# Kernel optimization log

Hardware: AMD Instinct MI355X
Metric: run time of the kernel (lower is better)

Reference implementation:

```python
import jax, jax.numpy as jnp
import numpy as np

DEPTH, HEADS, DIM_HEAD = 6, 8, 64
B, N, E = 2, 128, 160
NUM_ATOMS, NF = 100, 127
DIM = NF + 1                 # 128, node feature dim fed to transformer
INNER = HEADS * DIM_HEAD     # 512


def setup_inputs() -> dict:
    key = jax.random.key(0)
    ks = iter(jax.random.split(key, 40))
    f32 = jnp.float32
    def w(shape, scale=0.02):
        return jax.random.normal(next(ks), shape, dtype=f32) * scale
    inp = {
        "indices": jax.random.randint(next(ks), (B, N), 0, NUM_ATOMS),
        "coordinates": jax.random.normal(next(ks), (B, N, 3), dtype=f32),
        "bonds": jax.random.randint(next(ks), (E, 2), 0, N),
        "noise_level": jax.random.uniform(next(ks), (1,), dtype=f32),
        "atom_emb": w((NUM_ATOMS, NF), 1.0),
        "ln1_g": jnp.ones((DEPTH, DIM), f32), "ln1_b": jnp.zeros((DEPTH, DIM), f32),
        "Wq": w((DEPTH, DIM, INNER)), "bq": jnp.zeros((DEPTH, INNER), f32),
        "Wkv": w((DEPTH, DIM, 2 * INNER)), "bkv": jnp.zeros((DEPTH, 2 * INNER), f32),
        "We": w((DEPTH, 3, INNER)), "be": jnp.zeros((DEPTH, INNER), f32),
        "Wo": w((DEPTH, INNER, DIM)), "bo": jnp.zeros((DEPTH, DIM), f32),
        "Wg1": w((DEPTH, 3 * DIM, 1)),
        "ln2_g": jnp.ones((DEPTH, DIM), f32), "ln2_b": jnp.zeros((DEPTH, DIM), f32),
        "W1": w((DEPTH, DIM, 4 * DIM)), "b1": jnp.zeros((DEPTH, 4 * DIM), f32),
        "W2": w((DEPTH, 4 * DIM, DIM)), "b2": jnp.zeros((DEPTH, DIM), f32),
        "Wg2": w((DEPTH, 3 * DIM, 1)),
        "Wlin": w((DIM, 1)), "blin": jnp.zeros((1,), f32),
    }
    return inp


def _ln(x, g, b, eps=1e-5):
    m = jnp.mean(x, -1, keepdims=True)
    v = jnp.mean((x - m) ** 2, -1, keepdims=True)
    return (x - m) * jax.lax.rsqrt(v + eps) * g + b


def _gated_residual(x, res, Wg):
    # gate = sigmoid(Linear([x, res, x-res])); out = x*gate + res*(1-gate)
    gate = jax.nn.sigmoid(jnp.concatenate([x, res, x - res], -1) @ Wg)  # (B,N,1)
    return x * gate + res * (1.0 - gate)


def _forward(indices, bonds, coordinates, noise_level, atom_emb,
             ln1_g, ln1_b, Wq, bq, Wkv, bkv, We, be, Wo, bo, Wg1,
             ln2_g, ln2_b, W1, b1, W2, b2, Wg2, Wlin, blin):
    b, n = indices.shape
    # nodes_embedding: atom embedding + noise-level channel
    noise = jnp.broadcast_to(noise_level.reshape(1, 1, 1).astype(coordinates.dtype), (b, n, 1))
    nodes = jnp.concatenate([atom_emb[indices], noise], -1)  # (B,N,DIM)
    # edges_embedding: vectorized scatter of per-bond coordinate differences
    i, j = bonds[:, 0], bonds[:, 1]
    diff = coordinates[:, i] - coordinates[:, j]             # (B,E,3)
    edges = jnp.zeros((b, n, n, 3), coordinates.dtype)
    edges = edges.at[:, i, j].set(diff).at[:, j, i].set(-diff)

    scale = DIM_HEAD ** -0.5
    for l in range(DEPTH):
        # PreNorm + edge-biased attention (mask is all-ones -> no-op)
        xn = _ln(nodes, ln1_g[l], ln1_b[l])
        q = (xn @ Wq[l] + bq[l]).reshape(b, n, HEADS, DIM_HEAD)
        k, v = jnp.split(xn @ Wkv[l] + bkv[l], 2, -1)
        k = k.reshape(b, n, HEADS, DIM_HEAD)
        v = v.reshape(b, n, HEADS, DIM_HEAD)
        e = (edges @ We[l] + be[l]).reshape(b, n, n, HEADS, DIM_HEAD)
        kk = k[:, None] + e                                   # (B,i,j,H,D)
        vv = v[:, None] + e
        sim = jnp.einsum('bihd,bijhd->bijh', q, kk) * scale
        attn = jax.nn.softmax(sim, axis=2)                    # softmax over j
        out = jnp.einsum('bijh,bijhd->bihd', attn, vv).reshape(b, n, INNER)
        out = out @ Wo[l] + bo[l]
        nodes = _gated_residual(out, nodes, Wg1[l])
        # PreNorm + FeedForward (exact GELU, mult=4) + gated residual
        xn = _ln(nodes, ln2_g[l], ln2_b[l])
        ff = jax.nn.gelu(xn @ W1[l] + b1[l], approximate=False) @ W2[l] + b2[l]
        nodes = _gated_residual(ff, nodes, Wg2[l])
    return jnp.sum(nodes @ Wlin + blin)


def reference(indices, coordinates, bonds, noise_level, atom_emb,
              ln1_g, ln1_b, Wq, bq, Wkv, bkv, We, be, Wo, bo, Wg1,
              ln2_g, ln2_b, W1, b1, W2, b2, Wg2, Wlin, blin):
    return _forward(indices, bonds, coordinates, noise_level, atom_emb,
                    ln1_g, ln1_b, Wq, bq, Wkv, bkv, We, be, Wo, bo, Wg1,
                    ln2_g, ln2_b, W1, b1, W2, b2, Wg2, Wlin, blin)
```

## Files before the change

kernel.cpp:

```cpp
#include <hip/hip_runtime.h>
#include <hip/hip_fp16.h>
#include <math.h>

#define DEPTH 6
#define HEADS 8
#define BB    2
#define NN    128
#define EE    160
#define NF    127
#define DIMM  128
#define INNER 512
#define NNODE 256

__device__ __forceinline__ void gload16(const void* g, void* l) {
    __builtin_amdgcn_global_load_lds((const __attribute__((address_space(1))) void*)g,
                                     (__attribute__((address_space(3))) void*)l,
                                     16, 0, 0);
}

__device__ __forceinline__ void wait_vm0() { __builtin_amdgcn_s_waitcnt(0x0f70); }
__device__ __forceinline__ void wait_lgkm0() { __builtin_amdgcn_s_waitcnt(0xC07F); }

__device__ __forceinline__ void wstage16(const char* gslice, char* ldsslice, int ln) {
#pragma unroll
    for (int i = 0; i < 16; i++)
        gload16(gslice + i * 1024 + ln * 16, ldsslice + i * 1024);
}
__device__ __forceinline__ void wstage16s(const char* gslice, int rowstride,
                                          char* ldsslice, int ln) {
#pragma unroll
    for (int i = 0; i < 16; i++)
        gload16(gslice + (size_t)i * rowstride + ln * 16, ldsslice + i * 1024);
}

__device__ __forceinline__ void fma8h(float4& a0, float4& a1, float s, float4 raw) {
    const __half2* hp = (const __half2*)&raw;
    float2 p0 = __half22float2(hp[0]), p1 = __half22float2(hp[1]);
    float2 p2 = __half22float2(hp[2]), p3 = __half22float2(hp[3]);
    a0.x += s * p0.x; a0.y += s * p0.y; a0.z += s * p1.x; a0.w += s * p1.y;
    a1.x += s * p2.x; a1.y += s * p2.y; a1.z += s * p3.x; a1.w += s * p3.y;
}

__device__ __forceinline__ void gemv512(const float* act, const float* wbuf,
                                        float* s_part, int w, int ln) {
    float4 a0 = {0,0,0,0}, a1 = {0,0,0,0};
    const float4* w4 = (const float4*)wbuf;
#pragma unroll
    for (int r = 0; r < 16; r++)
        fma8h(a0, a1, act[w * 16 + r], w4[r * 64 + ln]);
    ((float4*)(s_part + w * 512))[ln * 2]     = a0;
    ((float4*)(s_part + w * 512))[ln * 2 + 1] = a1;
}

__device__ __forceinline__ void gemv128(const float* act, const float* wbuf,
                                        float* s_part, int w, int ln) {
    float2 acc = {0, 0};
#pragma unroll 8
    for (int r = 0; r < 64; r++) {
        float raw = wbuf[r * 64 + ln];
        float2 p = __half22float2(*(const __half2*)&raw);
        float a = act[w * 64 + r];
        acc.x += a * p.x; acc.y += a * p.y;
    }
    s_part[w * 128 + ln * 2]     = acc.x;
    s_part[w * 128 + ln * 2 + 1] = acc.y;
}

template <int N>
__device__ __forceinline__ void block_reduce_n(float* vals, float* sbuf) {
#pragma unroll
    for (int off = 32; off > 0; off >>= 1)
#pragma unroll
        for (int q = 0; q < N; q++) vals[q] += __shfl_xor(vals[q], off, 64);
    int wave = threadIdx.x >> 6;
    if ((threadIdx.x & 63) == 0)
#pragma unroll
        for (int q = 0; q < N; q++) sbuf[wave * N + q] = vals[q];
    __syncthreads();
#pragma unroll
    for (int q = 0; q < N; q++) {
        float r = 0.0f;
#pragma unroll
        for (int g = 0; g < 8; g++) r += sbuf[g * N + q];
        vals[q] = r;
    }
    __syncthreads();
}

__device__ __forceinline__ float gelu_exact(float a) {
    return 0.5f * a * (1.0f + erff(a * 0.70710678f));
}


__global__ __launch_bounds__(512) void k_cvt(const float* Wq, const float* Wkv,
                                             const float* Wo, const float* W1,
                                             const float* W2,
                                             __half* hWq, __half* hWkv, __half* hWo,
                                             __half* hW1, __half* hW2,
                                             const float* blin, float* out) {
    if (blockIdx.x == 0 && threadIdx.x == 0) out[0] = 256.0f * blin[0];
    int g = blockIdx.x * 512 + threadIdx.x;
    const float4* src; __half* dst; int off;
    if (g < 98304)       { src = (const float4*)Wq;  dst = hWq;  off = g; }
    else if (g < 294912) { src = (const float4*)Wkv; dst = hWkv; off = g - 98304; }
    else if (g < 393216) { src = (const float4*)Wo;  dst = hWo;  off = g - 294912; }
    else if (g < 491520) { src = (const float4*)W1;  dst = hW1;  off = g - 393216; }
    else                 { src = (const float4*)W2;  dst = hW2;  off = g - 491520; }
    float4 v = src[off];
    __half2* d2 = (__half2*)(dst + (size_t)off * 4);
    d2[0] = __floats2half2_rn(v.x, v.y);
    d2[1] = __floats2half2_rn(v.z, v.w);
}

__global__ __launch_bounds__(512, 1) void k_pre(const int* indices, const float* noise,
                                                const float* atom_emb,
                                                const float* ln1_g, const float* ln1_b,
                                                const __half* hWq, const float* bq,
                                                const __half* hWkv, const float* bkv,
                                                float* nodes, float* qb,
                                                __half* hk, __half* hv) {
    int bn = blockIdx.x;
    int t  = threadIdx.x;
    int d  = t & 127;
    bool own = (t < 128);
    int w = t >> 6, ln = t & 63;
    __shared__ float arena[32768];
    __shared__ float s_xn[128];
    __shared__ float s_red[48];
    __shared__ float s_part[4096];
    char*  lslice = (char*)arena + w * 16384;
    float* wbuf   = arena + w * 4096;

    const char* WqL  = (const char*)hWq;
    const char* WkvL = (const char*)hWkv;
    wstage16(WqL + w * 16384, lslice, ln);

    float nd = 0.0f;
    if (own) {
        int idx = indices[bn];
        nd = (d < NF) ? atom_emb[idx * NF + d] : noise[0];
        nodes[bn * DIMM + d] = nd;
    }
    float vals[2] = {own ? nd : 0.0f, own ? nd * nd : 0.0f};
    block_reduce_n<2>(vals, s_red);
    float m   = vals[0] * (1.0f / 128.0f);
    float var = vals[1] * (1.0f / 128.0f) - m * m;
    if (own) s_xn[d] = (nd - m) * rsqrtf(var + 1e-5f) * ln1_g[d] + ln1_b[d];
    __syncthreads();

    wait_vm0();
    gemv512(s_xn, wbuf, s_part, w, ln);
    wait_lgkm0();
    wstage16s(WkvL + (size_t)(w * 16) * 2048, 2048, lslice, ln);
    __syncthreads();
    {
        float q = bq[t];
#pragma unroll
        for (int g = 0; g < 8; g++) q += s_part[g * 512 + t];
        qb[(size_t)bn * INNER + t] = q;
    }
    __syncthreads();

    wait_vm0();
    gemv512(s_xn, wbuf, s_part, w, ln);
    wait_lgkm0();
    wstage16s(WkvL + (size_t)(w * 16) * 2048 + 1024, 2048, lslice, ln);
    __syncthreads();
    {
        float k = bkv[t];
#pragma unroll
        for (int g = 0; g < 8; g++) k += s_part[g * 512 + t];
        hk[(size_t)bn * INNER + t] = __float2half(k);
    }
    __syncthreads();

    wait_vm0();
    gemv512(s_xn, wbuf, s_part, w, ln);
    __syncthreads();
    {
        float v = bkv[INNER + t];
#pragma unroll
        for (int g = 0; g < 8; g++) v += s_part[g * 512 + t];
        hv[(size_t)bn * INNER + t] = __float2half(v);
    }
}

__global__ __launch_bounds__(512, 1) void k_layer(int l,
        const float* coords, const int* bonds,
        const float* We, const float* be,
        float* qb, const __half* hkin, const __half* hvin,
        __half* hkout, __half* hvout,
        const __half* hWo, const float* bo, const float* Wg1,
        const float* ln2_g, const float* ln2_b,
        const __half* hW1, const float* b1,
        const __half* hW2, const float* b2,
        const float* Wg2,
        const float* ln1_g, const float* ln1_b,
        const __half* hWq, const float* bq,
        const __half* hWkv, const float* bkv,
        float* nodes, const float* Wlin, float* out) {
    int bn = blockIdx.x;
    int b = bn >> 7, i = bn & 127;
    int t = threadIdx.x;
    int d = t & 127;
    bool own = (t < 128);
    int w = t >> 6, ln = t & 63;

    __shared__ float arena[32768];
    __shared__ float scoord[384];
    __shared__ float sedge[384];
    __shared__ int   sadj[128];
    __shared__ float s_l[64];
    __shared__ float s_ao[512];
    __shared__ float s_h[512];
    __shared__ float s_xn[128];
    __shared__ float s_red[48];
    __shared__ float s_part[4096];
    float* s_o = s_part;
    char*  lslice = (char*)arena + w * 16384;
    float* wbuf   = arena + w * 4096;

    const char* WoL  = (const char*)(hWo + (size_t)l * INNER * DIMM);
    const char* W1L  = (const char*)(hW1 + (size_t)l * DIMM * 4 * DIMM);
    const char* W2L  = (const char*)(hW2 + (size_t)l * 4 * DIMM * DIMM);
    const char* WqL  = (const char*)(hWq + (size_t)(l + 1) * DIMM * INNER);
    const char* WkvL = (const char*)(hWkv + (size_t)(l + 1) * DIMM * 2 * INNER);

    wstage16(WoL + w * 16384, lslice, ln);

    const float4* qR4 = (const float4*)(qb + (size_t)bn * INNER);
    const float4* WeR = (const float4*)(We + (size_t)l * 3 * INNER);
    float4 qa  = qR4[ln * 2],        qz  = qR4[ln * 2 + 1];
    float4 w0a = WeR[ln * 2],        w0z = WeR[ln * 2 + 1];
    float4 w1a = WeR[128 + ln * 2],  w1z = WeR[129 + ln * 2];
    float4 w2a = WeR[256 + ln * 2],  w2z = WeR[257 + ln * 2];
    float4 bea = ((const float4*)(be + (size_t)l * INNER))[ln * 2];
    float4 bez = ((const float4*)(be + (size_t)l * INNER))[ln * 2 + 1];
    float res = own ? nodes[bn * DIMM + d] : 0.0f;

    if (t < 3 * NN) scoord[t] = coords[b * 3 * NN + t];
    if (t < NN) sadj[t] = 0;
    __syncthreads();
    if (t < EE) {
        int e0 = bonds[2 * t], e1 = bonds[2 * t + 1];
        if (e0 == i) sadj[e1] = 1;
        if (e1 == i) sadj[e0] = 1;
    }
    __syncthreads();
    if (t < NN) {
        int j = t;
        float msk = sadj[j] ? 1.0f : 0.0f;
        sedge[3 * j + 0] = msk * (scoord[3 * i + 0] - scoord[3 * j + 0]);
        sedge[3 * j + 1] = msk * (scoord[3 * i + 1] - scoord[3 * j + 1]);
        sedge[3 * j + 2] = msk * (scoord[3 * i + 2] - scoord[3 * j + 2]);
    }
    __syncthreads();

    const float4* kR = (const float4*)(hkin + (size_t)b * NN * INNER);
    const float4* vR = (const float4*)(hvin + (size_t)b * NN * INNER);
    float l_run = 0.0f;
    float4 o0 = {0, 0, 0, 0}, o1 = {0, 0, 0, 0};
    int j0 = w * 16;
#pragma unroll
    for (int base = 0; base < 16; base += 4) {
        float4 kraw[4], vraw[4];
#pragma unroll
        for (int p = 0; p < 4; p++) {
            int j = j0 + base + p;
            kraw[p] = kR[j * 64 + ln];
            vraw[p] = vR[j * 64 + ln];
        }
#pragma unroll
        for (int p = 0; p < 4; p++) {
            int j = j0 + base + p;
            float ex = sedge[3 * j], ey = sedge[3 * j + 1], ez = sedge[3 * j + 2];
            float4 e0, e1;
            e0.x = bea.x + ex * w0a.x + ey * w1a.x + ez * w2a.x;
            e0.y = bea.y + ex * w0a.y + ey * w1a.y + ez * w2a.y;
            e0.z = bea.z + ex * w0a.z + ey * w1a.z + ez * w2a.z;
            e0.w = bea.w + ex * w0a.w + ey * w1a.w + ez * w2a.w;
            e1.x = bez.x + ex * w0z.x + ey * w1z.x + ez * w2z.x;
            e1.y = bez.y + ex * w0z.y + ey * w1z.y + ez * w2z.y;
            e1.z = bez.z + ex * w0z.z + ey * w1z.z + ez * w2z.z;
            e1.w = bez.w + ex * w0z.w + ey * w1z.w + ez * w2z.w;
            const __half2* kh = (const __half2*)&kraw[p];
            float2 k0 = __half22float2(kh[0]), k1 = __half22float2(kh[1]);
            float2 k2 = __half22float2(kh[2]), k3 = __half22float2(kh[3]);
            float s = qa.x * (k0.x + e0.x) + qa.y * (k0.y + e0.y)
                    + qa.z * (k1.x + e0.z) + qa.w * (k1.y + e0.w)
                    + qz.x * (k2.x + e1.x) + qz.y * (k2.y + e1.y)
                    + qz.z * (k3.x + e1.z) + qz.w * (k3.y + e1.w);
            s += __shfl_xor(s, 1, 64);
            s += __shfl_xor(s, 2, 64);
            s += __shfl_xor(s, 4, 64);
            float pp = __expf(s * 0.125f);
            const __half2* vh = (const __half2*)&vraw[p];
            float2 v0 = __half22float2(vh[0]), v1 = __half22float2(vh[1]);
            float2 v2 = __half22float2(vh[2]), v3 = __half22float2(vh[3]);
            l_run += pp;
            o0.x += pp * (v0.x + e0.x); o0.y += pp * (v0.y + e0.y);
            o0.z += pp * (v1.x + e0.z); o0.w += pp * (v1.y + e0.w);
            o1.x += pp * (v2.x + e1.x); o1.y += pp * (v2.y + e1.y);
            o1.z += pp * (v3.x + e1.z); o1.w += pp * (v3.y + e1.w);
        }
    }
    ((float4*)(s_o + w * 512))[ln * 2]     = o0;
    ((float4*)(s_o + w * 512))[ln * 2 + 1] = o1;
    if ((ln & 7) == 0) s_l[w * 8 + (ln >> 3)] = l_run;
    __syncthreads();
    {
        float o = 0.0f;
#pragma unroll
        for (int g = 0; g < 8; g++) o += s_o[g * 512 + t];
        int h = t >> 6;
        float lsum = 0.0f;
#pragma unroll
        for (int g = 0; g < 8; g++) lsum += s_l[g * 8 + h];
        s_ao[t] = o / lsum;
    }
    __syncthreads();

    wait_vm0();
    gemv128(s_ao, wbuf, s_part, w, ln);
    wait_lgkm0();
    wstage16(W1L + w * 16384, lslice, ln);
    __syncthreads();
    float x = 0.0f;
    if (own) {
        x = bo[l * DIMM + d];
#pragma unroll
        for (int g = 0; g < 8; g++) x += s_part[g * 128 + d];
    }

    const float* Wg1_l = Wg1 + l * 3 * DIMM;
    float n1;
    {
        float tex = own ? (x * Wg1_l[d] + res * Wg1_l[DIMM + d] + (x - res) * Wg1_l[2 * DIMM + d]) : 0.0f;
        float vals[6] = {tex,
                         own ? x : 0.0f, own ? x * x : 0.0f,
                         own ? x * res : 0.0f,
                         own ? res : 0.0f, own ? res * res : 0.0f};
        block_reduce_n<6>(vals, s_red);
        float g1 = 1.0f / (1.0f + __expf(-vals[0]));
        float sn  = g1 * vals[1] + (1.0f - g1) * vals[4];
        float sn2 = g1 * g1 * vals[2] + 2.0f * g1 * (1.0f - g1) * vals[3]
                  + (1.0f - g1) * (1.0f - g1) * vals[5];
        float m   = sn * (1.0f / 128.0f);
        float var = sn2 * (1.0f / 128.0f) - m * m;
        n1 = x * g1 + res * (1.0f - g1);
        if (own) s_xn[d] = (n1 - m) * rsqrtf(var + 1e-5f) * ln2_g[l * DIMM + d] + ln2_b[l * DIMM + d];
    }
    __syncthreads();

    wait_vm0();
    gemv512(s_xn, wbuf, s_part, w, ln);
    wait_lgkm0();
    wstage16(W2L + w * 16384, lslice, ln);
    __syncthreads();
    {
        float a = b1[l * 4 * DIMM + t];
#pragma unroll
        for (int g = 0; g < 8; g++) a += s_part[g * 512 + t];
        s_h[t] = gelu_exact(a);
    }
    __syncthreads();

    wait_vm0();
    gemv128(s_h, wbuf, s_part, w, ln);
    wait_lgkm0();
    if (l < DEPTH - 1) wstage16(WqL + w * 16384, lslice, ln);
    __syncthreads();
    float y = 0.0f;
    if (own) {
        y = b2[l * DIMM + d];
#pragma unroll
        for (int g = 0; g < 8; g++) y += s_part[g * 128 + d];
    }

    const float* Wg2_l = Wg2 + l * 3 * DIMM;
    if (l < DEPTH - 1) {
        float tex = own ? (y * Wg2_l[d] + n1 * Wg2_l[DIMM + d] + (y - n1) * Wg2_l[2 * DIMM + d]) : 0.0f;
        float vals[6] = {tex,
                         own ? y : 0.0f, own ? y * y : 0.0f,
                         own ? y * n1 : 0.0f,
                         own ? n1 : 0.0f, own ? n1 * n1 : 0.0f};
        block_reduce_n<6>(vals, s_red);
        float g2 = 1.0f / (1.0f + __expf(-vals[0]));
        float sn  = g2 * vals[1] + (1.0f - g2) * vals[4];
        float sn2 = g2 * g2 * vals[2] + 2.0f * g2 * (1.0f - g2) * vals[3]
                  + (1.0f - g2) * (1.0f - g2) * vals[5];
        float m   = sn * (1.0f / 128.0f);
        float var = sn2 * (1.0f / 128.0f) - m * m;
        float n2 = y * g2 + n1 * (1.0f - g2);
        if (own) {
            nodes[bn * DIMM + d] = n2;
            s_xn[d] = (n2 - m) * rsqrtf(var + 1e-5f) * ln1_g[(l + 1) * DIMM + d]
                    + ln1_b[(l + 1) * DIMM + d];
        }
        __syncthreads();

        wait_vm0();
        gemv512(s_xn, wbuf, s_part, w, ln);
        wait_lgkm0();
        wstage16s(WkvL + (size_t)(w * 16) * 2048, 2048, lslice, ln);
        __syncthreads();
        {
            float q = bq[(l + 1) * INNER + t];
#pragma unroll
            for (int g = 0; g < 8; g++) q += s_part[g * 512 + t];
            qb[(size_t)bn * INNER + t] = q;
        }
        __syncthreads();

        wait_vm0();
        gemv512(s_xn, wbuf, s_part, w, ln);
        wait_lgkm0();
        wstage16s(WkvL + (size_t)(w * 16) * 2048 + 1024, 2048, lslice, ln);
        __syncthreads();
        {
            float k = bkv[(l + 1) * 2 * INNER + t];
#pragma unroll
            for (int g = 0; g < 8; g++) k += s_part[g * 512 + t];
            hkout[(size_t)bn * INNER + t] = __float2half(k);
        }
        __syncthreads();

        wait_vm0();
        gemv512(s_xn, wbuf, s_part, w, ln);
        __syncthreads();
        {
            float v = bkv[(l + 1) * 2 * INNER + INNER + t];
#pragma unroll
            for (int g = 0; g < 8; g++) v += s_part[g * 512 + t];
            hvout[(size_t)bn * INNER + t] = __float2half(v);
        }
    } else {
        float wl = own ? Wlin[d] : 0.0f;
        float tex = own ? (y * Wg2_l[d] + n1 * Wg2_l[DIMM + d] + (y - n1) * Wg2_l[2 * DIMM + d]) : 0.0f;
        float vals[3] = {tex, y * wl, n1 * wl};
        block_reduce_n<3>(vals, s_red);
        float g2 = 1.0f / (1.0f + __expf(-vals[0]));
        float tot = g2 * vals[1] + (1.0f - g2) * vals[2];
        if (t == 0) atomicAdd(out, tot);
    }
}

extern "C" void kernel_launch(void* const* d_in, const int* in_sizes, int n_in,
                              void* d_out, int out_size, void* d_ws, size_t ws_size,
                              hipStream_t stream) {
    const int*   indices = (const int*)d_in[0];
    const float* coords  = (const float*)d_in[1];
    const int*   bonds   = (const int*)d_in[2];
    const float* noise   = (const float*)d_in[3];
    const float* atom_emb= (const float*)d_in[4];
    const float* ln1_g   = (const float*)d_in[5];
    const float* ln1_b   = (const float*)d_in[6];
    const float* Wq      = (const float*)d_in[7];
    const float* bq      = (const float*)d_in[8];
    const float* Wkv     = (const float*)d_in[9];
    const float* bkv     = (const float*)d_in[10];
    const float* We      = (const float*)d_in[11];
    const float* be      = (const float*)d_in[12];
    const float* Wo      = (const float*)d_in[13];
    const float* bo      = (const float*)d_in[14];
    const float* Wg1     = (const float*)d_in[15];
    const float* ln2_g   = (const float*)d_in[16];
    const float* ln2_b   = (const float*)d_in[17];
    const float* W1      = (const float*)d_in[18];
    const float* b1      = (const float*)d_in[19];
    const float* W2      = (const float*)d_in[20];
    const float* b2      = (const float*)d_in[21];
    const float* Wg2     = (const float*)d_in[22];
    const float* Wlin    = (const float*)d_in[23];
    const float* blin    = (const float*)d_in[24];

    float*  ws    = (float*)d_ws;
    float*  nodes = ws;
    float*  qb    = nodes + NNODE * DIMM;
    __half* hkb   = (__half*)(qb + NNODE * INNER);
    __half* hvb   = hkb + 2 * NNODE * INNER;
    __half* hWq   = hvb + 2 * NNODE * INNER;
    __half* hWkv  = hWq + DEPTH * DIMM * INNER;
    __half* hWo   = hWkv + DEPTH * DIMM * 2 * INNER;
    __half* hW1   = hWo + DEPTH * INNER * DIMM;
    __half* hW2   = hW1 + DEPTH * DIMM * 4 * DIMM;

    k_cvt<<<1152, 512, 0, stream>>>(Wq, Wkv, Wo, W1, W2, hWq, hWkv, hWo, hW1, hW2,
                                    blin, (float*)d_out);
    k_pre<<<NNODE, 512, 0, stream>>>(indices, noise, atom_emb, ln1_g, ln1_b,
                                     hWq, bq, hWkv, bkv, nodes, qb, hkb, hvb);
    for (int l = 0; l < DEPTH; l++) {
        const __half* hkin = hkb + (size_t)(l & 1) * NNODE * INNER;
        const __half* hvin = hvb + (size_t)(l & 1) * NNODE * INNER;
        __half* hkout = hkb + (size_t)((l + 1) & 1) * NNODE * INNER;
        __half* hvout = hvb + (size_t)((l + 1) & 1) * NNODE * INNER;
        k_layer<<<NNODE, 512, 0, stream>>>(l, coords, bonds, We, be,
                                           qb, hkin, hvin, hkout, hvout,
                                           hWo, bo, Wg1, ln2_g, ln2_b, hW1, b1, hW2, b2,
                                           Wg2, ln1_g, ln1_b, hWq, bq, hWkv, bkv,
                                           nodes, Wlin, (float*)d_out);
    }
}
```

Baseline: 270.1 us.

## Fuse all layers into one persistent kernel with grid barriers

Replaces the pre-kernel and six per-layer launches with a single persistent kernel of 256 blocks that loops over layers and synchronises with a software grid barrier on atomics. Node state and q now stay in registers and shared memory instead of round-tripping through global memory, and the next layer's Wo is prefetched during the QKV phase. The attention score switches to packed fp16 dot products (fdot2), and the edge term is skipped for unbonded pairs using a precomputed q·bias constant. The changes aim to cut launch overhead and redundant edge arithmetic. The barrier relies on all 256 blocks being co-resident, and q is rounded to fp16 for the score.

```diff
diff --git a/kernel.cpp b/kernel.cpp
--- a/kernel.cpp
+++ b/kernel.cpp
@@ -11,6 +11,23 @@
 #define DIMM  128
 #define INNER 512
 #define NNODE 256
+#define NBLK  256
+
+typedef _Float16 h2f16 __attribute__((ext_vector_type(2)));
+
+#if defined(__has_builtin)
+#if __has_builtin(__builtin_amdgcn_fdot2)
+#define HAVE_FDOT2 1
+#endif
+#endif
+
+__device__ __forceinline__ float fdot2f(h2f16 a, h2f16 b, float c) {
+#ifdef HAVE_FDOT2
+    return __builtin_amdgcn_fdot2(a, b, c, false);
+#else
+    return c + (float)a.x * (float)b.x + (float)a.y * (float)b.y;
+#endif
+}
 
 __device__ __forceinline__ void gload16(const void* g, void* l) {
     __builtin_amdgcn_global_load_lds((const __attribute__((address_space(1))) void*)g,
@@ -91,14 +108,37 @@
     return 0.5f * a * (1.0f + erff(a * 0.70710678f));
 }
 
+__device__ __forceinline__ void gridbar(unsigned* bar) {
+    __syncthreads();
+    if (threadIdx.x == 0) {
+        __threadfence();
+        unsigned g = __hip_atomic_load(&bar[1], __ATOMIC_RELAXED, __HIP_MEMORY_SCOPE_AGENT);
+        unsigned a = __hip_atomic_fetch_add(&bar[0], 1u, __ATOMIC_ACQ_REL, __HIP_MEMORY_SCOPE_AGENT);
+        if (a == NBLK - 1) {
+            __hip_atomic_store(&bar[0], 0u, __ATOMIC_RELAXED, __HIP_MEMORY_SCOPE_AGENT);
+            __hip_atomic_fetch_add(&bar[1], 1u, __ATOMIC_RELEASE, __HIP_MEMORY_SCOPE_AGENT);
+        } else {
+            while (__hip_atomic_load(&bar[1], __ATOMIC_ACQUIRE, __HIP_MEMORY_SCOPE_AGENT) == g)
+                __builtin_amdgcn_s_sleep(2);
+        }
+        __threadfence();
+    }
+    __syncthreads();
+}
+
 
 __global__ __launch_bounds__(512) void k_cvt(const float* Wq, const float* Wkv,
                                              const float* Wo, const float* W1,
                                              const float* W2,
                                              __half* hWq, __half* hWkv, __half* hWo,
                                              __half* hW1, __half* hW2,
-                                             const float* blin, float* out) {
-    if (blockIdx.x == 0 && threadIdx.x == 0) out[0] = 256.0f * blin[0];
+                                             const float* blin, float* out,
+                                             unsigned* bar) {
+    if (blockIdx.x == 0 && threadIdx.x == 0) {
+        out[0] = 256.0f * blin[0];
+        bar[0] = 0u;
+        bar[1] = 0u;
+    }
     int g = blockIdx.x * 512 + threadIdx.x;
     const float4* src; __half* dst; int off;
     if (g < 98304)       { src = (const float4*)Wq;  dst = hWq;  off = g; }
@@ -112,52 +152,22 @@
     d2[1] = __floats2half2_rn(v.z, v.w);
 }
 
-__global__ __launch_bounds__(512, 1) void k_pre(const int* indices, const float* noise,
-                                                const float* atom_emb,
-                                                const float* ln1_g, const float* ln1_b,
-                                                const __half* hWq, const float* bq,
-                                                const __half* hWkv, const float* bkv,
-                                                float* nodes, float* qb,
-                                                __half* hk, __half* hv) {
-    int bn = blockIdx.x;
-    int t  = threadIdx.x;
-    int d  = t & 127;
-    bool own = (t < 128);
-    int w = t >> 6, ln = t & 63;
-    __shared__ float arena[32768];
-    __shared__ float s_xn[128];
-    __shared__ float s_red[48];
-    __shared__ float s_part[4096];
-    char*  lslice = (char*)arena + w * 16384;
-    float* wbuf   = arena + w * 4096;
-
-    const char* WqL  = (const char*)hWq;
-    const char* WkvL = (const char*)hWkv;
-    wstage16(WqL + w * 16384, lslice, ln);
-
-    float nd = 0.0f;
-    if (own) {
-        int idx = indices[bn];
-        nd = (d < NF) ? atom_emb[idx * NF + d] : noise[0];
-        nodes[bn * DIMM + d] = nd;
-    }
-    float vals[2] = {own ? nd : 0.0f, own ? nd * nd : 0.0f};
-    block_reduce_n<2>(vals, s_red);
-    float m   = vals[0] * (1.0f / 128.0f);
-    float var = vals[1] * (1.0f / 128.0f) - m * m;
-    if (own) s_xn[d] = (nd - m) * rsqrtf(var + 1e-5f) * ln1_g[d] + ln1_b[d];
-    __syncthreads();
-
+__device__ __forceinline__ void qkv_phase(const float* s_xn, float* s_part, float* s_q,
+                                          char* lslice, float* wbuf,
+                                          const char* WkvL, const char* WoNextL,
+                                          const float* bq_l, const float* bkv_l,
+                                          __half* hkrow, __half* hvrow,
+                                          int w, int ln, int t) {
     wait_vm0();
     gemv512(s_xn, wbuf, s_part, w, ln);
     wait_lgkm0();
     wstage16s(WkvL + (size_t)(w * 16) * 2048, 2048, lslice, ln);
     __syncthreads();
     {
-        float q = bq[t];
+        float q = bq_l[t];
 #pragma unroll
         for (int g = 0; g < 8; g++) q += s_part[g * 512 + t];
-        qb[(size_t)bn * INNER + t] = q;
+        s_q[t] = q;
     }
     __syncthreads();
 
@@ -167,38 +177,36 @@
     wstage16s(WkvL + (size_t)(w * 16) * 2048 + 1024, 2048, lslice, ln);
     __syncthreads();
     {
-        float k = bkv[t];
+        float k = bkv_l[t];
 #pragma unroll
         for (int g = 0; g < 8; g++) k += s_part[g * 512 + t];
-        hk[(size_t)bn * INNER + t] = __float2half(k);
+        hkrow[t] = __float2half(k);
     }
     __syncthreads();
 
     wait_vm0();
     gemv512(s_xn, wbuf, s_part, w, ln);
+    wait_lgkm0();
+    wstage16(WoNextL + w * 16384, lslice, ln);
     __syncthreads();
     {
-        float v = bkv[INNER + t];
+        float v = bkv_l[INNER + t];
 #pragma unroll
         for (int g = 0; g < 8; g++) v += s_part[g * 512 + t];
-        hv[(size_t)bn * INNER + t] = __float2half(v);
-    }
-}
-
-__global__ __launch_bounds__(512, 1) void k_layer(int l,
-        const float* coords, const int* bonds,
+        hvrow[t] = __float2half(v);
+    }
+}
+
+__global__ __launch_bounds__(512, 1) void k_net(
+        const int* indices, const float* coords, const int* bonds, const float* noise,
+        const float* atom_emb, const float* ln1_g, const float* ln1_b,
+        const __half* hWq, const float* bq, const __half* hWkv, const float* bkv,
         const float* We, const float* be,
-        float* qb, const __half* hkin, const __half* hvin,
-        __half* hkout, __half* hvout,
         const __half* hWo, const float* bo, const float* Wg1,
         const float* ln2_g, const float* ln2_b,
-        const __half* hW1, const float* b1,
-        const __half* hW2, const float* b2,
-        const float* Wg2,
-        const float* ln1_g, const float* ln1_b,
-        const __half* hWq, const float* bq,
-        const __half* hWkv, const float* bkv,
-        float* nodes, const float* Wlin, float* out) {
+        const __half* hW1, const float* b1, const __half* hW2, const float* b2,
+        const float* Wg2, const float* Wlin, float* out,
+        __half* hkb, __half* hvb, unsigned* bar) {
     int bn = blockIdx.x;
     int b = bn >> 7, i = bn & 127;
     int t = threadIdx.x;
@@ -216,27 +224,12 @@
     __shared__ float s_xn[128];
     __shared__ float s_red[48];
     __shared__ float s_part[4096];
+    __shared__ float s_q[512];
     float* s_o = s_part;
     char*  lslice = (char*)arena + w * 16384;
     float* wbuf   = arena + w * 4096;
 
-    const char* WoL  = (const char*)(hWo + (size_t)l * INNER * DIMM);
-    const char* W1L  = (const char*)(hW1 + (size_t)l * DIMM * 4 * DIMM);
-    const char* W2L  = (const char*)(hW2 + (size_t)l * 4 * DIMM * DIMM);
-    const char* WqL  = (const char*)(hWq + (size_t)(l + 1) * DIMM * INNER);
-    const char* WkvL = (const char*)(hWkv + (size_t)(l + 1) * DIMM * 2 * INNER);
-
-    wstage16(WoL + w * 16384, lslice, ln);
-
-    const float4* qR4 = (const float4*)(qb + (size_t)bn * INNER);
-    const float4* WeR = (const float4*)(We + (size_t)l * 3 * INNER);
-    float4 qa  = qR4[ln * 2],        qz  = qR4[ln * 2 + 1];
-    float4 w0a = WeR[ln * 2],        w0z = WeR[ln * 2 + 1];
-    float4 w1a = WeR[128 + ln * 2],  w1z = WeR[129 + ln * 2];
-    float4 w2a = WeR[256 + ln * 2],  w2z = WeR[257 + ln * 2];
-    float4 bea = ((const float4*)(be + (size_t)l * INNER))[ln * 2];
-    float4 bez = ((const float4*)(be + (size_t)l * INNER))[ln * 2 + 1];
-    float res = own ? nodes[bn * DIMM + d] : 0.0f;
+    wstage16((const char*)hWq + w * 16384, lslice, ln);
 
     if (t < 3 * NN) scoord[t] = coords[b * 3 * NN + t];
     if (t < NN) sadj[t] = 0;
@@ -254,194 +247,216 @@
         sedge[3 * j + 1] = msk * (scoord[3 * i + 1] - scoord[3 * j + 1]);
         sedge[3 * j + 2] = msk * (scoord[3 * i + 2] - scoord[3 * j + 2]);
     }
-    __syncthreads();
-
-    const float4* kR = (const float4*)(hkin + (size_t)b * NN * INNER);
-    const float4* vR = (const float4*)(hvin + (size_t)b * NN * INNER);
-    float l_run = 0.0f;
-    float4 o0 = {0, 0, 0, 0}, o1 = {0, 0, 0, 0};
-    int j0 = w * 16;
-#pragma unroll
-    for (int base = 0; base < 16; base += 4) {
-        float4 kraw[4], vraw[4];
-#pragma unroll
-        for (int p = 0; p < 4; p++) {
-            int j = j0 + base + p;
-            kraw[p] = kR[j * 64 + ln];
-            vraw[p] = vR[j * 64 + ln];
-        }
-#pragma unroll
-        for (int p = 0; p < 4; p++) {
-            int j = j0 + base + p;
-            float ex = sedge[3 * j], ey = sedge[3 * j + 1], ez = sedge[3 * j + 2];
-            float4 e0, e1;
-            e0.x = bea.x + ex * w0a.x + ey * w1a.x + ez * w2a.x;
-            e0.y = bea.y + ex * w0a.y + ey * w1a.y + ez * w2a.y;
-            e0.z = bea.z + ex * w0a.z + ey * w1a.z + ez * w2a.z;
-            e0.w = bea.w + ex * w0a.w + ey * w1a.w + ez * w2a.w;
-            e1.x = bez.x + ex * w0z.x + ey * w1z.x + ez * w2z.x;
-            e1.y = bez.y + ex * w0z.y + ey * w1z.y + ez * w2z.y;
-            e1.z = bez.z + ex * w0z.z + ey * w1z.z + ez * w2z.z;
-            e1.w = bez.w + ex * w0z.w + ey * w1z.w + ez * w2z.w;
-            const __half2* kh = (const __half2*)&kraw[p];
-            float2 k0 = __half22float2(kh[0]), k1 = __half22float2(kh[1]);
-            float2 k2 = __half22float2(kh[2]), k3 = __half22float2(kh[3]);
-            float s = qa.x * (k0.x + e0.x) + qa.y * (k0.y + e0.y)
-                    + qa.z * (k1.x + e0.z) + qa.w * (k1.y + e0.w)
-                    + qz.x * (k2.x + e1.x) + qz.y * (k2.y + e1.y)
-                    + qz.z * (k3.x + e1.z) + qz.w * (k3.y + e1.w);
-            s += __shfl_xor(s, 1, 64);
-            s += __shfl_xor(s, 2, 64);
-            s += __shfl_xor(s, 4, 64);
-            float pp = __expf(s * 0.125f);
-            const __half2* vh = (const __half2*)&vraw[p];
-            float2 v0 = __half22float2(vh[0]), v1 = __half22float2(vh[1]);
-            float2 v2 = __half22float2(vh[2]), v3 = __half22float2(vh[3]);
-            l_run += pp;
-            o0.x += pp * (v0.x + e0.x); o0.y += pp * (v0.y + e0.y);
-            o0.z += pp * (v1.x + e0.z); o0.w += pp * (v1.y + e0.w);
-            o1.x += pp * (v2.x + e1.x); o1.y += pp * (v2.y + e1.y);
-            o1.z += pp * (v3.x + e1.z); o1.w += pp * (v3.y + e1.w);
-        }
-    }
-    ((float4*)(s_o + w * 512))[ln * 2]     = o0;
-    ((float4*)(s_o + w * 512))[ln * 2 + 1] = o1;
-    if ((ln & 7) == 0) s_l[w * 8 + (ln >> 3)] = l_run;
-    __syncthreads();
+
+    float res = 0.0f;
+    if (own) {
+        int idx = indices[bn];
+        res = (d < NF) ? atom_emb[idx * NF + d] : noise[0];
+    }
     {
-        float o = 0.0f;
-#pragma unroll
-        for (int g = 0; g < 8; g++) o += s_o[g * 512 + t];
-        int h = t >> 6;
-        float lsum = 0.0f;
-#pragma unroll
-        for (int g = 0; g < 8; g++) lsum += s_l[g * 8 + h];
-        s_ao[t] = o / lsum;
-    }
-    __syncthreads();
-
-    wait_vm0();
-    gemv128(s_ao, wbuf, s_part, w, ln);
-    wait_lgkm0();
-    wstage16(W1L + w * 16384, lslice, ln);
-    __syncthreads();
-    float x = 0.0f;
-    if (own) {
-        x = bo[l * DIMM + d];
-#pragma unroll
-        for (int g = 0; g < 8; g++) x += s_part[g * 128 + d];
-    }
-
-    const float* Wg1_l = Wg1 + l * 3 * DIMM;
-    float n1;
-    {
-        float tex = own ? (x * Wg1_l[d] + res * Wg1_l[DIMM + d] + (x - res) * Wg1_l[2 * DIMM + d]) : 0.0f;
-        float vals[6] = {tex,
-                         own ? x : 0.0f, own ? x * x : 0.0f,
-                         own ? x * res : 0.0f,
-                         own ? res : 0.0f, own ? res * res : 0.0f};
-        block_reduce_n<6>(vals, s_red);
-        float g1 = 1.0f / (1.0f + __expf(-vals[0]));
-        float sn  = g1 * vals[1] + (1.0f - g1) * vals[4];
-        float sn2 = g1 * g1 * vals[2] + 2.0f * g1 * (1.0f - g1) * vals[3]
-                  + (1.0f - g1) * (1.0f - g1) * vals[5];
-        float m   = sn * (1.0f / 128.0f);
-        float var = sn2 * (1.0f / 128.0f) - m * m;
-        n1 = x * g1 + res * (1.0f - g1);
-        if (own) s_xn[d] = (n1 - m) * rsqrtf(var + 1e-5f) * ln2_g[l * DIMM + d] + ln2_b[l * DIMM + d];
-    }
-    __syncthreads();
-
-    wait_vm0();
-    gemv512(s_xn, wbuf, s_part, w, ln);
-    wait_lgkm0();
-    wstage16(W2L + w * 16384, lslice, ln);
-    __syncthreads();
-    {
-        float a = b1[l * 4 * DIMM + t];
-#pragma unroll
-        for (int g = 0; g < 8; g++) a += s_part[g * 512 + t];
-        s_h[t] = gelu_exact(a);
-    }
-    __syncthreads();
-
-    wait_vm0();
-    gemv128(s_h, wbuf, s_part, w, ln);
-    wait_lgkm0();
-    if (l < DEPTH - 1) wstage16(WqL + w * 16384, lslice, ln);
-    __syncthreads();
-    float y = 0.0f;
-    if (own) {
-        y = b2[l * DIMM + d];
-#pragma unroll
-        for (int g = 0; g < 8; g++) y += s_part[g * 128 + d];
-    }
-
-    const float* Wg2_l = Wg2 + l * 3 * DIMM;
-    if (l < DEPTH - 1) {
-        float tex = own ? (y * Wg2_l[d] + n1 * Wg2_l[DIMM + d] + (y - n1) * Wg2_l[2 * DIMM + d]) : 0.0f;
-        float vals[6] = {tex,
-                         own ? y : 0.0f, own ? y * y : 0.0f,
-                         own ? y * n1 : 0.0f,
-                         own ? n1 : 0.0f, own ? n1 * n1 : 0.0f};
-        block_reduce_n<6>(vals, s_red);
-        float g2 = 1.0f / (1.0f + __expf(-vals[0]));
-        float sn  = g2 * vals[1] + (1.0f - g2) * vals[4];
-        float sn2 = g2 * g2 * vals[2] + 2.0f * g2 * (1.0f - g2) * vals[3]
-                  + (1.0f - g2) * (1.0f - g2) * vals[5];
-        float m   = sn * (1.0f / 128.0f);
-        float var = sn2 * (1.0f / 128.0f) - m * m;
-        float n2 = y * g2 + n1 * (1.0f - g2);
+        float vals[2] = {own ? res : 0.0f, own ? res * res : 0.0f};
+        block_reduce_n<2>(vals, s_red);
+        float m   = vals[0] * (1.0f / 128.0f);
+        float var = vals[1] * (1.0f / 128.0f) - m * m;
+        if (own) s_xn[d] = (res - m) * rsqrtf(var + 1e-5f) * ln1_g[d] + ln1_b[d];
+    }
+    __syncthreads();
+
+    qkv_phase(s_xn, s_part, s_q, lslice, wbuf,
+              (const char*)hWkv, (const char*)hWo, bq, bkv,
+              hkb + (size_t)bn * INNER, hvb + (size_t)bn * INNER, w, ln, t);
+    gridbar(bar);
+
+    for (int l = 0; l < DEPTH; l++) {
+        const float4* kR = (const float4*)(hkb + (size_t)(l & 1) * NNODE * INNER
+                                               + (size_t)b * NN * INNER);
+        const float4* vR = (const float4*)(hvb + (size_t)(l & 1) * NNODE * INNER
+                                               + (size_t)b * NN * INNER);
+        const float4* WeR = (const float4*)(We + (size_t)l * 3 * INNER);
+        const float4* beR = (const float4*)(be + (size_t)l * INNER);
+
+        float4 qa = ((const float4*)s_q)[ln * 2], qz = ((const float4*)s_q)[ln * 2 + 1];
+        float4 w0a = WeR[ln * 2],       w0z = WeR[ln * 2 + 1];
+        float4 w1a = WeR[128 + ln * 2], w1z = WeR[129 + ln * 2];
+        float4 w2a = WeR[256 + ln * 2], w2z = WeR[257 + ln * 2];
+        float4 bea = beR[ln * 2],       bez = beR[ln * 2 + 1];
+        h2f16 qh0 = {(_Float16)qa.x, (_Float16)qa.y};
+        h2f16 qh1 = {(_Float16)qa.z, (_Float16)qa.w};
+        h2f16 qh2 = {(_Float16)qz.x, (_Float16)qz.y};
+        h2f16 qh3 = {(_Float16)qz.z, (_Float16)qz.w};
+        float c = qa.x * bea.x + qa.y * bea.y + qa.z * bea.z + qa.w * bea.w
+                + qz.x * bez.x + qz.y * bez.y + qz.z * bez.z + qz.w * bez.w;
+        c += __shfl_xor(c, 1, 64); c += __shfl_xor(c, 2, 64); c += __shfl_xor(c, 4, 64);
+
+        float l_run = 0.0f, S_nb = 0.0f;
+        float4 o0 = {0, 0, 0, 0}, o1 = {0, 0, 0, 0};
+        int j0 = w * 16;
+#pragma unroll
+        for (int base = 0; base < 16; base += 4) {
+            float4 kraw[4], vraw[4];
+#pragma unroll
+            for (int p = 0; p < 4; p++) {
+                int j = j0 + base + p;
+                kraw[p] = kR[j * 64 + ln];
+                vraw[p] = vR[j * 64 + ln];
+            }
+#pragma unroll
+            for (int p = 0; p < 4; p++) {
+                int j = j0 + base + p;
+                const h2f16* kh = (const h2f16*)&kraw[p];
+                float s = fdot2f(qh0, kh[0],
+                          fdot2f(qh1, kh[1],
+                          fdot2f(qh2, kh[2],
+                          fdot2f(qh3, kh[3], 0.0f))));
+                bool bonded = (sadj[j] != 0);
+                float4 e0, e1;
+                if (bonded) {
+                    float ex = sedge[3 * j], ey = sedge[3 * j + 1], ez = sedge[3 * j + 2];
+                    e0.x = bea.x + ex * w0a.x + ey * w1a.x + ez * w2a.x;
+                    e0.y = bea.y + ex * w0a.y + ey * w1a.y + ez * w2a.y;
+                    e0.z = bea.z + ex * w0a.z + ey * w1a.z + ez * w2a.z;
+                    e0.w = bea.w + ex * w0a.w + ey * w1a.w + ez * w2a.w;
+                    e1.x = bez.x + ex * w0z.x + ey * w1z.x + ez * w2z.x;
+                    e1.y = bez.y + ex * w0z.y + ey * w1z.y + ez * w2z.y;
+                    e1.z = bez.z + ex * w0z.z + ey * w1z.z + ez * w2z.z;
+                    e1.w = bez.w + ex * w0z.w + ey * w1z.w + ez * w2z.w;
+                    s += qa.x * e0.x + qa.y * e0.y + qa.z * e0.z + qa.w * e0.w
+                       + qz.x * e1.x + qz.y * e1.y + qz.z * e1.z + qz.w * e1.w;
+                }
+                s += __shfl_xor(s, 1, 64);
+                s += __shfl_xor(s, 2, 64);
+                s += __shfl_xor(s, 4, 64);
+                if (!bonded) s += c;
+                float pp = __expf(s * 0.125f);
+                l_run += pp;
+                const __half2* vh = (const __half2*)&vraw[p];
+                float2 v0 = __half22float2(vh[0]), v1 = __half22float2(vh[1]);
+                float2 v2 = __half22float2(vh[2]), v3 = __half22float2(vh[3]);
+                o0.x += pp * v0.x; o0.y += pp * v0.y; o0.z += pp * v1.x; o0.w += pp * v1.y;
+                o1.x += pp * v2.x; o1.y += pp * v2.y; o1.z += pp * v3.x; o1.w += pp * v3.y;
+                if (bonded) {
+                    o0.x += pp * e0.x; o0.y += pp * e0.y; o0.z += pp * e0.z; o0.w += pp * e0.w;
+                    o1.x += pp * e1.x; o1.y += pp * e1.y; o1.z += pp * e1.z; o1.w += pp * e1.w;
+                } else S_nb += pp;
+            }
+        }
+        o0.x += S_nb * bea.x; o0.y += S_nb * bea.y; o0.z += S_nb * bea.z; o0.w += S_nb * bea.w;
+        o1.x += S_nb * bez.x; o1.y += S_nb * bez.y; o1.z += S_nb * bez.z; o1.w += S_nb * bez.w;
+        ((float4*)(s_o + w * 512))[ln * 2]     = o0;
+        ((float4*)(s_o + w * 512))[ln * 2 + 1] = o1;
+        if ((ln & 7) == 0) s_l[w * 8 + (ln >> 3)] = l_run;
+        __syncthreads();
+        {
+            float o = 0.0f;
+#pragma unroll
+            for (int g = 0; g < 8; g++) o += s_o[g * 512 + t];
+            int h = t >> 6;
+            float lsum = 0.0f;
+#pragma unroll
+            for (int g = 0; g < 8; g++) lsum += s_l[g * 8 + h];
+            s_ao[t] = o / lsum;
+        }
+        __syncthreads();
+
+        wait_vm0();
+        gemv128(s_ao, wbuf, s_part, w, ln);
+        wait_lgkm0();
+        wstage16((const char*)hW1 + (size_t)l * 131072 + w * 16384, lslice, ln);
+        __syncthreads();
+        float x = 0.0f;
         if (own) {
-            nodes[bn * DIMM + d] = n2;
-            s_xn[d] = (n2 - m) * rsqrtf(var + 1e-5f) * ln1_g[(l + 1) * DIMM + d]
-                    + ln1_b[(l + 1) * DIMM + d];
+            x = bo[l * DIMM + d];
+#pragma unroll
+            for (int g = 0; g < 8; g++) x += s_part[g * 128 + d];
+        }
+
+        const float* Wg1_l = Wg1 + l * 3 * DIMM;
+        float n1;
+        {
+            float tex = own ? (x * Wg1_l[d] + res * Wg1_l[DIMM + d]
+                               + (x - res) * Wg1_l[2 * DIMM + d]) : 0.0f;
+            float vals[6] = {tex,
+                             own ? x : 0.0f, own ? x * x : 0.0f,
+                             own ? x * res : 0.0f,
+                             own ? res : 0.0f, own ? res * res : 0.0f};
+            block_reduce_n<6>(vals, s_red);
+            float g1 = 1.0f / (1.0f + __expf(-vals[0]));
+            float sn  = g1 * vals[1] + (1.0f - g1) * vals[4];
+            float sn2 = g1 * g1 * vals[2] + 2.0f * g1 * (1.0f - g1) * vals[3]
+                      + (1.0f - g1) * (1.0f - g1) * vals[5];
+            float m   = sn * (1.0f / 128.0f);
+            float var = sn2 * (1.0f / 128.0f) - m * m;
+            n1 = x * g1 + res * (1.0f - g1);
+            if (own) s_xn[d] = (n1 - m) * rsqrtf(var + 1e-5f) * ln2_g[l * DIMM + d]
+                             + ln2_b[l * DIMM + d];
         }
         __syncthreads();
 
         wait_vm0();
         gemv512(s_xn, wbuf, s_part, w, ln);
         wait_lgkm0();
-        wstage16s(WkvL + (size_t)(w * 16) * 2048, 2048, lslice, ln);
+        wstage16((const char*)hW2 + (size_t)l * 131072 + w * 16384, lslice, ln);
         __syncthreads();
         {
-            float q = bq[(l + 1) * INNER + t];
-#pragma unroll
-            for (int g = 0; g < 8; g++) q += s_part[g * 512 + t];
-            qb[(size_t)bn * INNER + t] = q;
+            float a = b1[l * 4 * DIMM + t];
+#pragma unroll
+            for (int g = 0; g < 8; g++) a += s_part[g * 512 + t];
+            s_h[t] = gelu_exact(a);
         }
         __syncthreads();
 
         wait_vm0();
-        gemv512(s_xn, wbuf, s_part, w, ln);
+        gemv128(s_h, wbuf, s_part, w, ln);
         wait_lgkm0();
-        wstage16s(WkvL + (size_t)(w * 16) * 2048 + 1024, 2048, lslice, ln);
-        __syncthreads();
-        {
-            float k = bkv[(l + 1) * 2 * INNER + t];
-#pragma unroll
-            for (int g = 0; g < 8; g++) k += s_part[g * 512 + t];
-            hkout[(size_t)bn * INNER + t] = __float2half(k);
-        }
-        __syncthreads();
-
-        wait_vm0();
-        gemv512(s_xn, wbuf, s_part, w, ln);
-        __syncthreads();
-        {
-            float v = bkv[(l + 1) * 2 * INNER + INNER + t];
-#pragma unroll
-            for (int g = 0; g < 8; g++) v += s_part[g * 512 + t];
-            hvout[(size_t)bn * INNER + t] = __float2half(v);
-        }
-    } else {
-        float wl = own ? Wlin[d] : 0.0f;
-        float tex = own ? (y * Wg2_l[d] + n1 * Wg2_l[DIMM + d] + (y - n1) * Wg2_l[2 * DIMM + d]) : 0.0f;
-        float vals[3] = {tex, y * wl, n1 * wl};
-        block_reduce_n<3>(vals, s_red);
-        float g2 = 1.0f / (1.0f + __expf(-vals[0]));
-        float tot = g2 * vals[1] + (1.0f - g2) * vals[2];
-        if (t == 0) atomicAdd(out, tot);
+        if (l < DEPTH - 1)
+            wstage16((const char*)hWq + (size_t)(l + 1) * 131072 + w * 16384, lslice, ln);
+        __syncthreads();
+        float y = 0.0f;
+        if (own) {
+            y = b2[l * DIMM + d];
+#pragma unroll
+            for (int g = 0; g < 8; g++) y += s_part[g * 128 + d];
+        }
+
+        const float* Wg2_l = Wg2 + l * 3 * DIMM;
+        if (l < DEPTH - 1) {
+            float tex = own ? (y * Wg2_l[d] + n1 * Wg2_l[DIMM + d]
+                               + (y - n1) * Wg2_l[2 * DIMM + d]) : 0.0f;
+            float vals[6] = {tex,
+                             own ? y : 0.0f, own ? y * y : 0.0f,
+                             own ? y * n1 : 0.0f,
+                             own ? n1 : 0.0f, own ? n1 * n1 : 0.0f};
+            block_reduce_n<6>(vals, s_red);
+            float g2 = 1.0f / (1.0f + __expf(-vals[0]));
+            float sn  = g2 * vals[1] + (1.0f - g2) * vals[4];
+            float sn2 = g2 * g2 * vals[2] + 2.0f * g2 * (1.0f - g2) * vals[3]
+                      + (1.0f - g2) * (1.0f - g2) * vals[5];
+            float m   = sn * (1.0f / 128.0f);
+            float var = sn2 * (1.0f / 128.0f) - m * m;
+            float n2 = y * g2 + n1 * (1.0f - g2);
+            res = n2;
+            if (own) s_xn[d] = (n2 - m) * rsqrtf(var + 1e-5f) * ln1_g[(l + 1) * DIMM + d]
+                             + ln1_b[(l + 1) * DIMM + d];
+            __syncthreads();
+
+            qkv_phase(s_xn, s_part, s_q, lslice, wbuf,
+                      (const char*)hWkv + (size_t)(l + 1) * 262144,
+                      (const char*)hWo + (size_t)(l + 1) * 131072,
+                      bq + (size_t)(l + 1) * INNER, bkv + (size_t)(l + 1) * 2 * INNER,
+                      hkb + (size_t)((l + 1) & 1) * NNODE * INNER + (size_t)bn * INNER,
+                      hvb + (size_t)((l + 1) & 1) * NNODE * INNER + (size_t)bn * INNER,
+                      w, ln, t);
+            gridbar(bar);
+        } else {
+            float wl = own ? Wlin[d] : 0.0f;
+            float tex = own ? (y * Wg2_l[d] + n1 * Wg2_l[DIMM + d]
+                               + (y - n1) * Wg2_l[2 * DIMM + d]) : 0.0f;
+            float vals[3] = {tex, y * wl, n1 * wl};
+            block_reduce_n<3>(vals, s_red);
+            float g2 = 1.0f / (1.0f + __expf(-vals[0]));
+            float tot = g2 * vals[1] + (1.0f - g2) * vals[2];
+            if (t == 0) atomicAdd(out, tot);
+        }
     }
 }
 
@@ -474,30 +489,20 @@
     const float* Wlin    = (const float*)d_in[23];
     const float* blin    = (const float*)d_in[24];
 
-    float*  ws    = (float*)d_ws;
-    float*  nodes = ws;
-    float*  qb    = nodes + NNODE * DIMM;
-    __half* hkb   = (__half*)(qb + NNODE * INNER);
-    __half* hvb   = hkb + 2 * NNODE * INNER;
-    __half* hWq   = hvb + 2 * NNODE * INNER;
-    __half* hWkv  = hWq + DEPTH * DIMM * INNER;
-    __half* hWo   = hWkv + DEPTH * DIMM * 2 * INNER;
-    __half* hW1   = hWo + DEPTH * INNER * DIMM;
-    __half* hW2   = hW1 + DEPTH * DIMM * 4 * DIMM;
+    float*    ws  = (float*)d_ws;
+    unsigned* bar = (unsigned*)ws;
+    __half* hkb  = (__half*)(ws + 16);
+    __half* hvb  = hkb + 2 * NNODE * INNER;
+    __half* hWq  = hvb + 2 * NNODE * INNER;
+    __half* hWkv = hWq + DEPTH * DIMM * INNER;
+    __half* hWo  = hWkv + DEPTH * DIMM * 2 * INNER;
+    __half* hW1  = hWo + DEPTH * INNER * DIMM;
+    __half* hW2  = hW1 + DEPTH * DIMM * 4 * DIMM;
 
     k_cvt<<<1152, 512, 0, stream>>>(Wq, Wkv, Wo, W1, W2, hWq, hWkv, hWo, hW1, hW2,
-                                    blin, (float*)d_out);
-    k_pre<<<NNODE, 512, 0, stream>>>(indices, noise, atom_emb, ln1_g, ln1_b,
-                                     hWq, bq, hWkv, bkv, nodes, qb, hkb, hvb);
-    for (int l = 0; l < DEPTH; l++) {
-        const __half* hkin = hkb + (size_t)(l & 1) * NNODE * INNER;
-        const __half* hvin = hvb + (size_t)(l & 1) * NNODE * INNER;
-        __half* hkout = hkb + (size_t)((l + 1) & 1) * NNODE * INNER;
-        __half* hvout = hvb + (size_t)((l + 1) & 1) * NNODE * INNER;
-        k_layer<<<NNODE, 512, 0, stream>>>(l, coords, bonds, We, be,
-                                           qb, hkin, hvin, hkout, hvout,
-                                           hWo, bo, Wg1, ln2_g, ln2_b, hW1, b1, hW2, b2,
-                                           Wg2, ln1_g, ln1_b, hWq, bq, hWkv, bkv,
-                                           nodes, Wlin, (float*)d_out);
-    }
-}
+                                    blin, (float*)d_out, bar);
+    k_net<<<NBLK, 512, 0, stream>>>(indices, coords, bonds, noise, atom_emb,
+                                    ln1_g, ln1_b, hWq, bq, hWkv, bkv, We, be,
+                                    hWo, bo, Wg1, ln2_g, ln2_b, hW1, b1, hW2, b2,
+                                    Wg2, Wlin, (float*)d_out, hkb, hvb, bar);
+}
```

Result: slower. 412.7 us (+52.8%).
